# Optimization experiments

Hardware: AMD Instinct MI355X
Metric: run time of the kernel (lower is better)

## Reference

```python
import jax, jax.numpy as jnp
import numpy as np

N, C, TX, TY = 32, 256, 1024, 1024


def setup_inputs() -> dict:
    key = jax.random.key(0)
    ks = jax.random.split(key, 9)
    s = 1.0 / np.sqrt(C)
    return {
        "Q": jax.random.normal(ks[0], (N, C, TY), dtype=jnp.float32),
        "K": jax.random.normal(ks[1], (N, C, TX), dtype=jnp.float32),
        "V": jax.random.normal(ks[2], (N, C, TX), dtype=jnp.float32),
        "Wq": jax.random.normal(ks[3], (C, C), dtype=jnp.float32) * s,
        "bq": jax.random.normal(ks[4], (C,), dtype=jnp.float32) * 0.01,
        "Wk": jax.random.normal(ks[5], (C, C), dtype=jnp.float32) * s,
        "bk": jax.random.normal(ks[6], (C,), dtype=jnp.float32) * 0.01,
        "Wv": jax.random.normal(ks[7], (C, C), dtype=jnp.float32) * s,
        "bv": jax.random.normal(ks[8], (C,), dtype=jnp.float32) * 0.01,
    }


def _proj_tanh(W, b, x):
    # 1x1 conv over channels: (C_out, C_in) x (N, C_in, T) -> (N, C_out, T)
    return jnp.tanh(jnp.einsum("oc,nct->not", W, x) + b[None, :, None])


def reference(Q, K, V, Wq, bq, Wk, bk, Wv, bv):
    d_k = Q.shape[1]
    Qp = _proj_tanh(Wq, bq, Q)  # (N, C, Ty)
    Kp = _proj_tanh(Wk, bk, K)  # (N, C, Tx)
    Vp = _proj_tanh(Wv, bv, V)  # (N, C, Tx)
    scores = jnp.einsum("ncs,nct->nst", Kp, Qp) / jnp.sqrt(
        jnp.asarray(d_k, dtype=Q.dtype)
    )  # (N, Tx, Ty)
    A = jax.nn.softmax(scores, axis=1)  # softmax over Tx (dim=1)
    R = jnp.einsum("ncs,nst->nct", Vp, A)  # (N, C, Ty)
    return (R, A)
```

## Files before the change

### kernel.cpp

```cpp
#include <hip/hip_runtime.h>
#include <stdint.h>

#define N_B 32
#define C_D 256
#define T_D 1024

typedef unsigned short u16;
typedef __attribute__((ext_vector_type(8))) short short8;
typedef __attribute__((ext_vector_type(4))) float f32x4;

__device__ __forceinline__ u16 f2bf(float f) {
    unsigned x = __float_as_uint(f);
    return (u16)((x + 0x7fffu + ((x >> 16) & 1u)) >> 16);
}

__device__ __forceinline__ void gld16(const void* g, void* l) {
    __builtin_amdgcn_global_load_lds(
        (const __attribute__((address_space(1))) uint32_t*)g,
        (__attribute__((address_space(3))) uint32_t*)l, 16, 0, 0);
}

__global__ __launch_bounds__(256) void conv_w(const float* __restrict__ w0,
                                              const float* __restrict__ w1,
                                              const float* __restrict__ w2,
                                              u16* __restrict__ o0,
                                              u16* __restrict__ o1,
                                              u16* __restrict__ o2) {
    const float* in = blockIdx.y == 0 ? w0 : (blockIdx.y == 1 ? w1 : w2);
    u16* out       = blockIdx.y == 0 ? o0 : (blockIdx.y == 1 ? o1 : o2);
    int i = blockIdx.x * 256 + threadIdx.x;
    out[i] = f2bf(in[i]);
}

__device__ __forceinline__ void stage_tr(const float* __restrict__ src,
                                         u16* __restrict__ sm, int tid) {
    const int sr2 = tid >> 4;
    const int tt8 = (tid & 15) * 8;
    float4 v0 = *(const float4*)(src);
    float4 v1 = *(const float4*)(src + 4);
    float4 w0 = *(const float4*)(src + T_D);
    float4 w1 = *(const float4*)(src + T_D + 4);
    float a[8] = {v0.x, v0.y, v0.z, v0.w, v1.x, v1.y, v1.z, v1.w};
    float b[8] = {w0.x, w0.y, w0.z, w0.w, w1.x, w1.y, w1.z, w1.w};
    const int kk = sr2 * 2;
#pragma unroll
    for (int j = 0; j < 8; ++j) {
        const int t  = tt8 + j;
        const int ks = kk ^ (((t >> 4) & 3) << 3);
        uint32_t pk = (uint32_t)f2bf(a[j]) | ((uint32_t)f2bf(b[j]) << 16);
        *(uint32_t*)(sm + t * 32 + ks) = pk;
    }
}

template <bool TRA, bool TRB, int EPI, bool F32OUT>
__global__ __launch_bounds__(256) void gemm_t(
        const void* __restrict__ Av, const void* __restrict__ Bv,
        const float* __restrict__ bias, void* __restrict__ OutV,
        int Kdim, int ldo, long sA, long sB, long sO, float scale)
{
    __shared__ __align__(16) u16 smA[128 * 32];
    __shared__ __align__(16) u16 smB[128 * 32];

    const int nb = blockIdx.z;
    const int n0 = blockIdx.x * 128;
    const int m0 = blockIdx.y * 128;
    const int tid = threadIdx.x;

    const int srow = tid >> 2;
    const int sk8  = (tid & 3) * 8;
    const int sr2  = tid >> 4;
    const int tt8  = (tid & 15) * 8;

    const u16* gA0 = nullptr; const u16* gA1 = nullptr;
    const float* tA = nullptr;
    if constexpr (TRA) {
        tA = (const float*)Av + (size_t)nb * sA + (size_t)(sr2 * 2) * T_D + m0 + tt8;
    } else {
        const u16* Ab = (const u16*)Av + (size_t)nb * sA;
        gA0 = Ab + (size_t)(m0 + srow) * Kdim + sk8;
        gA1 = gA0 + (size_t)64 * Kdim;
    }
    const u16* gB0 = nullptr; const u16* gB1 = nullptr;
    const float* tB = nullptr;
    if constexpr (TRB) {
        tB = (const float*)Bv + (size_t)nb * sB + (size_t)(sr2 * 2) * T_D + n0 + tt8;
    } else {
        const u16* Bb = (const u16*)Bv + (size_t)nb * sB;
        gB0 = Bb + (size_t)(n0 + srow) * Kdim + sk8;
        gB1 = gB0 + (size_t)64 * Kdim;
    }
    u16* lA0 = smA + tid * 8; u16* lA1 = smA + 2048 + tid * 8;
    u16* lB0 = smB + tid * 8; u16* lB1 = smB + 2048 + tid * 8;

    const int lane = tid & 63;
    const int w    = tid >> 6;
    const int wm   = (w >> 1) * 64;
    const int wn   = (w & 1) * 64;
    const int l15  = lane & 15;
    const int quad = lane >> 4;

    f32x4 acc[4][4];
#pragma unroll
    for (int i = 0; i < 4; ++i)
#pragma unroll
        for (int j = 0; j < 4; ++j) acc[i][j] = (f32x4){0.f, 0.f, 0.f, 0.f};

    for (int kb = 0; kb < Kdim; kb += 32) {
        if constexpr (TRA) {
            stage_tr(tA + (size_t)kb * T_D, smA, tid);
        } else {
            gld16(gA0 + kb, lA0);
            gld16(gA1 + kb, lA1);
        }
        if constexpr (TRB) {
            stage_tr(tB + (size_t)kb * T_D, smB, tid);
        } else {
            gld16(gB0 + kb, lB0);
            gld16(gB1 + kb, lB1);
        }
        __syncthreads();
        short8 af[4], bfr[4];
#pragma unroll
        for (int i = 0; i < 4; ++i) {
            const int ra = wm + i * 16 + l15;
            const int ca = TRA ? ((quad ^ ((ra >> 4) & 3)) * 8) : (quad * 8);
            af[i] = *(const short8*)(smA + ra * 32 + ca);
            const int rb = wn + i * 16 + l15;
            const int cb = TRB ? ((quad ^ ((rb >> 4) & 3)) * 8) : (quad * 8);
            bfr[i] = *(const short8*)(smB + rb * 32 + cb);
        }
#pragma unroll
        for (int mi = 0; mi < 4; ++mi)
#pragma unroll
            for (int ni = 0; ni < 4; ++ni)
                acc[mi][ni] = __builtin_amdgcn_mfma_f32_16x16x32_bf16(
                        af[mi], bfr[ni], acc[mi][ni], 0, 0, 0);
        __syncthreads();
    }

#pragma unroll
    for (int mi = 0; mi < 4; ++mi) {
        const int mb = m0 + wm + mi * 16 + quad * 4;
#pragma unroll
        for (int r = 0; r < 4; ++r) {
            const int m = mb + r;
            float bm = 0.f;
            if (EPI == 2) bm = bias[m];
#pragma unroll
            for (int ni = 0; ni < 4; ++ni) {
                const int nn = n0 + wn + ni * 16 + l15;
                float v = acc[mi][ni][r] * scale;
                if (EPI == 1) v = tanhf(v + bias[nn]);
                if (EPI == 2) v = tanhf(v + bm);
                if (F32OUT)
                    ((float*)OutV)[(size_t)nb * sO + (size_t)m * ldo + nn] = v;
                else
                    ((u16*)OutV)[(size_t)nb * sO + (size_t)m * ldo + nn] = f2bf(v);
            }
        }
    }
}

__global__ __launch_bounds__(256) void softmax_cols(float* __restrict__ S) {
    __shared__ float pm[16][64];
    __shared__ float pl[16][64];
    __shared__ float fM[64];
    __shared__ float fR[64];
    const int n   = blockIdx.y;
    const int t0  = blockIdx.x * 64;
    const int tid = threadIdx.x;
    const int g   = tid >> 4;
    const int ci  = (tid & 15) * 4;
    float* A = S + (size_t)n * T_D * T_D + t0 + ci;
    float* p = A + (size_t)g * 64 * T_D;

    float m[4] = {-1e30f, -1e30f, -1e30f, -1e30f};
    float l[4] = {0.f, 0.f, 0.f, 0.f};
#pragma unroll 8
    for (int s = 0; s < 64; ++s) {
        float4 v = *(const float4*)(p + (size_t)s * T_D);
        float x[4] = {v.x, v.y, v.z, v.w};
#pragma unroll
        for (int j = 0; j < 4; ++j) {
            float nm = fmaxf(m[j], x[j]);
            l[j] = l[j] * __expf(m[j] - nm) + __expf(x[j] - nm);
            m[j] = nm;
        }
    }
#pragma unroll
    for (int j = 0; j < 4; ++j) { pm[g][ci + j] = m[j]; pl[g][ci + j] = l[j]; }
    __syncthreads();
    if (tid < 64) {
        float M = -1e30f;
#pragma unroll
        for (int g2 = 0; g2 < 16; ++g2) M = fmaxf(M, pm[g2][tid]);
        float L = 0.f;
#pragma unroll
        for (int g2 = 0; g2 < 16; ++g2) L += pl[g2][tid] * __expf(pm[g2][tid] - M);
        fM[tid] = M;
        fR[tid] = 1.0f / L;
    }
    __syncthreads();
    float M[4], R[4];
#pragma unroll
    for (int j = 0; j < 4; ++j) { M[j] = fM[ci + j]; R[j] = fR[ci + j]; }
#pragma unroll 8
    for (int s = 0; s < 64; ++s) {
        float4 v = *(const float4*)(p + (size_t)s * T_D);
        v.x = __expf(v.x - M[0]) * R[0];
        v.y = __expf(v.y - M[1]) * R[1];
        v.z = __expf(v.z - M[2]) * R[2];
        v.w = __expf(v.w - M[3]) * R[3];
        *(float4*)(p + (size_t)s * T_D) = v;
    }
}

extern "C" void kernel_launch(void* const* d_in, const int* in_sizes, int n_in,
                              void* d_out, int out_size, void* d_ws, size_t ws_size,
                              hipStream_t stream) {
    const float* Qf = (const float*)d_in[0];
    const float* Kf = (const float*)d_in[1];
    const float* Vf = (const float*)d_in[2];
    const float* Wq = (const float*)d_in[3];
    const float* bq = (const float*)d_in[4];
    const float* Wk = (const float*)d_in[5];
    const float* bk = (const float*)d_in[6];
    const float* Wv = (const float*)d_in[7];
    const float* bv = (const float*)d_in[8];

    float* Rout = (float*)d_out;
    float* Aout = Rout + (size_t)N_B * C_D * T_D;

    u16* QpT = (u16*)Rout;
    u16* KpT = (u16*)Rout + 8388608;
    u16* Wqb = (u16*)Aout;
    u16* Wkb = Wqb + 65536;
    u16* Wvb = Wkb + 65536;
    u16* Vp  = (u16*)d_in[0];

    dim3 blk(256);
    const long sX = (long)C_D * T_D;
    const long sS = (long)T_D * T_D;

    conv_w<<<dim3(256, 3), blk, 0, stream>>>(Wq, Wk, Wv, Wqb, Wkb, Wvb);

    gemm_t<true, false, 1, false><<<dim3(2, 8, N_B), blk, 0, stream>>>(
            Qf, Wqb, bq, QpT, C_D, C_D, sX, 0, sX, 1.0f);
    gemm_t<true, false, 1, false><<<dim3(2, 8, N_B), blk, 0, stream>>>(
            Kf, Wkb, bk, KpT, C_D, C_D, sX, 0, sX, 1.0f);
    gemm_t<false, true, 2, false><<<dim3(8, 2, N_B), blk, 0, stream>>>(
            Wvb, Vf, bv, Vp, C_D, T_D, 0, sX, sX, 1.0f);

    gemm_t<false, false, 0, true><<<dim3(8, 8, N_B), blk, 0, stream>>>(
            KpT, QpT, nullptr, Aout, C_D, T_D, sX, sX, sS, 0.0625f);

    softmax_cols<<<dim3(16, N_B), blk, 0, stream>>>(Aout);

    gemm_t<false, true, 0, true><<<dim3(8, 2, N_B), blk, 0, stream>>>(
            Vp, Aout, nullptr, Rout, T_D, T_D, sX, sS, sX, 1.0f);
}
```

Baseline: 418.8 us.

## Fuse column softmax statistics into score GEMM and normalization into AV GEMM

The score GEMM epilogue now computes per-tile column max and sum-exp partials. A small merge kernel combines them into final max and reciprocal-sum. The final AV GEMM applies the exp/normalize while staging A, and its blockIdx.y==0 blocks write the normalized A out. This removes the separate multi-pass softmax over the 128MB score matrix, at the cost of recomputing exp in the two m-blocks of the AV GEMM and needing a large workspace. Fallback paths use a standalone normalize pass or the old softmax when workspace is small.

```diff
diff --git a/kernel.cpp b/kernel.cpp
--- a/kernel.cpp
+++ b/kernel.cpp
@@ -18,6 +18,12 @@
     __builtin_amdgcn_global_load_lds(
         (const __attribute__((address_space(1))) uint32_t*)g,
         (__attribute__((address_space(3))) uint32_t*)l, 16, 0, 0);
+}
+
+__device__ __forceinline__ void comb(float& m, float& l, float m2, float l2) {
+    float M = fmaxf(m, m2);
+    l = l * __expf(m - M) + l2 * __expf(m2 - M);
+    m = M;
 }
 
 __global__ __launch_bounds__(256) void conv_w(const float* __restrict__ w0,
@@ -32,8 +38,11 @@
     out[i] = f2bf(in[i]);
 }
 
+template <bool NORM>
 __device__ __forceinline__ void stage_tr(const float* __restrict__ src,
-                                         u16* __restrict__ sm, int tid) {
+                                         u16* __restrict__ sm, int tid,
+                                         const float* Mv, const float* Rv,
+                                         float* adst, bool awr) {
     const int sr2 = tid >> 4;
     const int tt8 = (tid & 15) * 8;
     float4 v0 = *(const float4*)(src);
@@ -42,6 +51,19 @@
     float4 w1 = *(const float4*)(src + T_D + 4);
     float a[8] = {v0.x, v0.y, v0.z, v0.w, v1.x, v1.y, v1.z, v1.w};
     float b[8] = {w0.x, w0.y, w0.z, w0.w, w1.x, w1.y, w1.z, w1.w};
+    if constexpr (NORM) {
+#pragma unroll
+        for (int j = 0; j < 8; ++j) {
+            a[j] = __expf(a[j] - Mv[j]) * Rv[j];
+            b[j] = __expf(b[j] - Mv[j]) * Rv[j];
+        }
+        if (awr) {
+            ((float4*)adst)[0]         = make_float4(a[0], a[1], a[2], a[3]);
+            ((float4*)adst)[1]         = make_float4(a[4], a[5], a[6], a[7]);
+            ((float4*)(adst + T_D))[0] = make_float4(b[0], b[1], b[2], b[3]);
+            ((float4*)(adst + T_D))[1] = make_float4(b[4], b[5], b[6], b[7]);
+        }
+    }
     const int kk = sr2 * 2;
 #pragma unroll
     for (int j = 0; j < 8; ++j) {
@@ -52,11 +74,14 @@
     }
 }
 
-template <bool TRA, bool TRB, int EPI, bool F32OUT>
+template <bool TRA, bool TRB, int EPI, bool F32OUT, bool NORM>
 __global__ __launch_bounds__(256) void gemm_t(
         const void* __restrict__ Av, const void* __restrict__ Bv,
         const float* __restrict__ bias, void* __restrict__ OutV,
-        int Kdim, int ldo, long sA, long sB, long sO, float scale)
+        int Kdim, int ldo, long sA, long sB, long sO, float scale,
+        float* __restrict__ Pm, float* __restrict__ Pl,
+        const float* __restrict__ Mf, const float* __restrict__ Rl,
+        float* __restrict__ Aw)
 {
     __shared__ __align__(16) u16 smA[128 * 32];
     __shared__ __align__(16) u16 smB[128 * 32];
@@ -92,6 +117,19 @@
     u16* lA0 = smA + tid * 8; u16* lA1 = smA + 2048 + tid * 8;
     u16* lB0 = smB + tid * 8; u16* lB1 = smB + 2048 + tid * 8;
 
+    float Mv[8], Rv[8];
+    float* awbase = nullptr;
+    bool awr = false;
+    if constexpr (NORM) {
+#pragma unroll
+        for (int j = 0; j < 8; ++j) {
+            Mv[j] = Mf[(size_t)nb * T_D + n0 + tt8 + j];
+            Rv[j] = Rl[(size_t)nb * T_D + n0 + tt8 + j];
+        }
+        awbase = Aw + (size_t)nb * sB + (size_t)(sr2 * 2) * T_D + n0 + tt8;
+        awr = (blockIdx.y == 0);
+    }
+
     const int lane = tid & 63;
     const int w    = tid >> 6;
     const int wm   = (w >> 1) * 64;
@@ -107,13 +145,17 @@
 
     for (int kb = 0; kb < Kdim; kb += 32) {
         if constexpr (TRA) {
-            stage_tr(tA + (size_t)kb * T_D, smA, tid);
+            stage_tr<false>(tA + (size_t)kb * T_D, smA, tid, nullptr, nullptr, nullptr, false);
         } else {
             gld16(gA0 + kb, lA0);
             gld16(gA1 + kb, lA1);
         }
         if constexpr (TRB) {
-            stage_tr(tB + (size_t)kb * T_D, smB, tid);
+            if constexpr (NORM)
+                stage_tr<true>(tB + (size_t)kb * T_D, smB, tid, Mv, Rv,
+                               awbase + (size_t)kb * T_D, awr);
+            else
+                stage_tr<false>(tB + (size_t)kb * T_D, smB, tid, nullptr, nullptr, nullptr, false);
         } else {
             gld16(gB0 + kb, lB0);
             gld16(gB1 + kb, lB1);
@@ -138,27 +180,117 @@
         __syncthreads();
     }
 
-#pragma unroll
-    for (int mi = 0; mi < 4; ++mi) {
-        const int mb = m0 + wm + mi * 16 + quad * 4;
-#pragma unroll
-        for (int r = 0; r < 4; ++r) {
-            const int m = mb + r;
-            float bm = 0.f;
-            if (EPI == 2) bm = bias[m];
+    if constexpr (EPI == 3) {
+        float pmv[4] = {-1e30f, -1e30f, -1e30f, -1e30f};
+        float plv[4] = {0.f, 0.f, 0.f, 0.f};
+#pragma unroll
+        for (int mi = 0; mi < 4; ++mi) {
+            const int mb = m0 + wm + mi * 16 + quad * 4;
+#pragma unroll
+            for (int r = 0; r < 4; ++r) {
+                const int m = mb + r;
+#pragma unroll
+                for (int ni = 0; ni < 4; ++ni) {
+                    const int nn = n0 + wn + ni * 16 + l15;
+                    float v = acc[mi][ni][r] * scale;
+                    ((float*)OutV)[(size_t)nb * sO + (size_t)m * ldo + nn] = v;
+                    pmv[ni] = fmaxf(pmv[ni], v);
+                }
+            }
+        }
+#pragma unroll
+        for (int ni = 0; ni < 4; ++ni) {
+            float s = 0.f;
+#pragma unroll
+            for (int mi = 0; mi < 4; ++mi)
+#pragma unroll
+                for (int r = 0; r < 4; ++r)
+                    s += __expf(acc[mi][ni][r] * scale - pmv[ni]);
+            plv[ni] = s;
+        }
+#pragma unroll
+        for (int ni = 0; ni < 4; ++ni) {
+            float m = pmv[ni], l = plv[ni];
+            float m2 = __shfl_xor(m, 16), l2 = __shfl_xor(l, 16);
+            comb(m, l, m2, l2);
+            m2 = __shfl_xor(m, 32); l2 = __shfl_xor(l, 32);
+            comb(m, l, m2, l2);
+            pmv[ni] = m; plv[ni] = l;
+        }
+        __shared__ float red_m[4][64];
+        __shared__ float red_l[4][64];
+        if (quad == 0) {
 #pragma unroll
             for (int ni = 0; ni < 4; ++ni) {
-                const int nn = n0 + wn + ni * 16 + l15;
-                float v = acc[mi][ni][r] * scale;
-                if (EPI == 1) v = tanhf(v + bias[nn]);
-                if (EPI == 2) v = tanhf(v + bm);
-                if (F32OUT)
-                    ((float*)OutV)[(size_t)nb * sO + (size_t)m * ldo + nn] = v;
-                else
-                    ((u16*)OutV)[(size_t)nb * sO + (size_t)m * ldo + nn] = f2bf(v);
+                red_m[w][ni * 16 + l15] = pmv[ni];
+                red_l[w][ni * 16 + l15] = plv[ni];
             }
         }
-    }
+        __syncthreads();
+        if (tid < 128) {
+            const int half = tid >> 6, cc = tid & 63;
+            float m = red_m[half][cc], l = red_l[half][cc];
+            comb(m, l, red_m[half + 2][cc], red_l[half + 2][cc]);
+            const size_t pi = ((size_t)nb * 8 + blockIdx.y) * T_D + n0 + tid;
+            Pm[pi] = m; Pl[pi] = l;
+        }
+    } else {
+#pragma unroll
+        for (int mi = 0; mi < 4; ++mi) {
+            const int mb = m0 + wm + mi * 16 + quad * 4;
+#pragma unroll
+            for (int r = 0; r < 4; ++r) {
+                const int m = mb + r;
+                float bm = 0.f;
+                if (EPI == 2) bm = bias[m];
+#pragma unroll
+                for (int ni = 0; ni < 4; ++ni) {
+                    const int nn = n0 + wn + ni * 16 + l15;
+                    float v = acc[mi][ni][r] * scale;
+                    if (EPI == 1) v = tanhf(v + bias[nn]);
+                    if (EPI == 2) v = tanhf(v + bm);
+                    if (F32OUT)
+                        ((float*)OutV)[(size_t)nb * sO + (size_t)m * ldo + nn] = v;
+                    else
+                        ((u16*)OutV)[(size_t)nb * sO + (size_t)m * ldo + nn] = f2bf(v);
+                }
+            }
+        }
+    }
+}
+
+__global__ __launch_bounds__(256) void merge_ml(const float* __restrict__ Pm,
+                                                const float* __restrict__ Pl,
+                                                float* __restrict__ Mf,
+                                                float* __restrict__ Rl) {
+    const int i = blockIdx.x * 256 + threadIdx.x;
+    const int n = i >> 10, t = i & (T_D - 1);
+    const float* pm = Pm + (size_t)n * 8 * T_D + t;
+    const float* pl = Pl + (size_t)n * 8 * T_D + t;
+    float M = -1e30f;
+#pragma unroll
+    for (int j = 0; j < 8; ++j) M = fmaxf(M, pm[(size_t)j * T_D]);
+    float L = 0.f;
+#pragma unroll
+    for (int j = 0; j < 8; ++j) L += pl[(size_t)j * T_D] * __expf(pm[(size_t)j * T_D] - M);
+    Mf[i] = M;
+    Rl[i] = 1.0f / L;
+}
+
+__global__ __launch_bounds__(256) void norm_a(float* __restrict__ S,
+                                              const float* __restrict__ Mf,
+                                              const float* __restrict__ Rl) {
+    const size_t i = ((size_t)blockIdx.x * 256 + threadIdx.x) * 4;
+    const int n = (int)(i >> 20);
+    const int t = (int)(i & (T_D - 1));
+    float4 M = *(const float4*)(Mf + (size_t)n * T_D + t);
+    float4 R = *(const float4*)(Rl + (size_t)n * T_D + t);
+    float4 v = *(float4*)(S + i);
+    v.x = __expf(v.x - M.x) * R.x;
+    v.y = __expf(v.y - M.y) * R.y;
+    v.z = __expf(v.z - M.z) * R.z;
+    v.w = __expf(v.w - M.w) * R.w;
+    *(float4*)(S + i) = v;
 }
 
 __global__ __launch_bounds__(256) void softmax_cols(float* __restrict__ S) {
@@ -242,20 +374,57 @@
     const long sX = (long)C_D * T_D;
     const long sS = (long)T_D * T_D;
 
+    const size_t elemsS = (size_t)N_B * T_D * T_D;
+    const size_t elemsP = (size_t)N_B * 8 * T_D;
+    const size_t elemsM = (size_t)N_B * T_D;
+    const size_t needA = (elemsS + 2 * elemsP + 2 * elemsM) * 4;
+    const size_t needB = (2 * elemsP + 2 * elemsM) * 4;
+
     conv_w<<<dim3(256, 3), blk, 0, stream>>>(Wq, Wk, Wv, Wqb, Wkb, Wvb);
 
-    gemm_t<true, false, 1, false><<<dim3(2, 8, N_B), blk, 0, stream>>>(
-            Qf, Wqb, bq, QpT, C_D, C_D, sX, 0, sX, 1.0f);
-    gemm_t<true, false, 1, false><<<dim3(2, 8, N_B), blk, 0, stream>>>(
-            Kf, Wkb, bk, KpT, C_D, C_D, sX, 0, sX, 1.0f);
-    gemm_t<false, true, 2, false><<<dim3(8, 2, N_B), blk, 0, stream>>>(
-            Wvb, Vf, bv, Vp, C_D, T_D, 0, sX, sX, 1.0f);
-
-    gemm_t<false, false, 0, true><<<dim3(8, 8, N_B), blk, 0, stream>>>(
-            KpT, QpT, nullptr, Aout, C_D, T_D, sX, sX, sS, 0.0625f);
-
-    softmax_cols<<<dim3(16, N_B), blk, 0, stream>>>(Aout);
-
-    gemm_t<false, true, 0, true><<<dim3(8, 2, N_B), blk, 0, stream>>>(
-            Vp, Aout, nullptr, Rout, T_D, T_D, sX, sS, sX, 1.0f);
-}
+    gemm_t<true, false, 1, false, false><<<dim3(2, 8, N_B), blk, 0, stream>>>(
+            Qf, Wqb, bq, QpT, C_D, C_D, sX, 0, sX, 1.0f,
+            nullptr, nullptr, nullptr, nullptr, nullptr);
+    gemm_t<true, false, 1, false, false><<<dim3(2, 8, N_B), blk, 0, stream>>>(
+            Kf, Wkb, bk, KpT, C_D, C_D, sX, 0, sX, 1.0f,
+            nullptr, nullptr, nullptr, nullptr, nullptr);
+    gemm_t<false, true, 2, false, false><<<dim3(8, 2, N_B), blk, 0, stream>>>(
+            Wvb, Vf, bv, Vp, C_D, T_D, 0, sX, sX, 1.0f,
+            nullptr, nullptr, nullptr, nullptr, nullptr);
+
+    if (ws_size >= needA) {
+        float* Sws = (float*)d_ws;
+        float* Pm  = Sws + elemsS;
+        float* Pl  = Pm + elemsP;
+        float* Mf  = Pl + elemsP;
+        float* Rl  = Mf + elemsM;
+        gemm_t<false, false, 3, true, false><<<dim3(8, 8, N_B), blk, 0, stream>>>(
+                KpT, QpT, nullptr, Sws, C_D, T_D, sX, sX, sS, 0.0625f,
+                Pm, Pl, nullptr, nullptr, nullptr);
+        merge_ml<<<dim3(128), blk, 0, stream>>>(Pm, Pl, Mf, Rl);
+        gemm_t<false, true, 0, true, true><<<dim3(8, 2, N_B), blk, 0, stream>>>(
+                Vp, Sws, nullptr, Rout, T_D, T_D, sX, sS, sX, 1.0f,
+                nullptr, nullptr, Mf, Rl, Aout);
+    } else if (ws_size >= needB) {
+        float* Pm = (float*)d_ws;
+        float* Pl = Pm + elemsP;
+        float* Mf = Pl + elemsP;
+        float* Rl = Mf + elemsM;
+        gemm_t<false, false, 3, true, false><<<dim3(8, 8, N_B), blk, 0, stream>>>(
+                KpT, QpT, nullptr, Aout, C_D, T_D, sX, sX, sS, 0.0625f,
+                Pm, Pl, nullptr, nullptr, nullptr);
+        merge_ml<<<dim3(128), blk, 0, stream>>>(Pm, Pl, Mf, Rl);
+        norm_a<<<dim3(32768), blk, 0, stream>>>(Aout, Mf, Rl);
+        gemm_t<false, true, 0, true, false><<<dim3(8, 2, N_B), blk, 0, stream>>>(
+                Vp, Aout, nullptr, Rout, T_D, T_D, sX, sS, sX, 1.0f,
+                nullptr, nullptr, nullptr, nullptr, nullptr);
+    } else {
+        gemm_t<false, false, 0, true, false><<<dim3(8, 8, N_B), blk, 0, stream>>>(
+                KpT, QpT, nullptr, Aout, C_D, T_D, sX, sX, sS, 0.0625f,
+                nullptr, nullptr, nullptr, nullptr, nullptr);
+        softmax_cols<<<dim3(16, N_B), blk, 0, stream>>>(Aout);
+        gemm_t<false, true, 0, true, false><<<dim3(8, 2, N_B), blk, 0, stream>>>(
+                Vp, Aout, nullptr, Rout, T_D, T_D, sX, sS, sX, 1.0f,
+                nullptr, nullptr, nullptr, nullptr, nullptr);
+    }
+}
```

Result: no change. 418.8 us (-0.0%).

## Fuse scores, column softmax and value GEMM into one attention kernel

Applied to the files above, without the earlier changes.

Replaces the separate score GEMM, column-softmax pass and final A·V GEMM with one kernel. Each block computes all 1024 scores for a 32-column query slice, reduces max/sum across waves in LDS, writes normalized A once, and keeps a bf16 copy of P in LDS for the V multiply. This removes the read-modify-write passes over the large fp32 A matrix. It also merges the Q and K projections into one launch, adds an XOR swizzle to the non-transposed LDS tiles, and writes R to a scratch input buffer that is then copied to the output, which costs an extra copy pass.

```diff
diff --git a/kernel.cpp b/kernel.cpp
--- a/kernel.cpp
+++ b/kernel.cpp
@@ -4,6 +4,7 @@
 #define N_B 32
 #define C_D 256
 #define T_D 1024
+#define QB 32
 
 typedef unsigned short u16;
 typedef __attribute__((ext_vector_type(8))) short short8;
@@ -18,6 +19,12 @@
     __builtin_amdgcn_global_load_lds(
         (const __attribute__((address_space(1))) uint32_t*)g,
         (__attribute__((address_space(3))) uint32_t*)l, 16, 0, 0);
+}
+
+__device__ __forceinline__ void comb(float& m, float& l, float m2, float l2) {
+    float M = fmaxf(m, m2);
+    l = l * __expf(m - M) + l2 * __expf(m2 - M);
+    m = M;
 }
 
 __global__ __launch_bounds__(256) void conv_w(const float* __restrict__ w0,
@@ -33,9 +40,8 @@
 }
 
 __device__ __forceinline__ void stage_tr(const float* __restrict__ src,
-                                         u16* __restrict__ sm, int tid) {
-    const int sr2 = tid >> 4;
-    const int tt8 = (tid & 15) * 8;
+                                         u16* __restrict__ sm,
+                                         int sr2, int tt8) {
     float4 v0 = *(const float4*)(src);
     float4 v1 = *(const float4*)(src + 4);
     float4 w0 = *(const float4*)(src + T_D);
@@ -52,22 +58,28 @@
     }
 }
 
-template <bool TRA, bool TRB, int EPI, bool F32OUT>
+template <bool TRA, bool TRB, int EPI, bool DUAL>
 __global__ __launch_bounds__(256) void gemm_t(
         const void* __restrict__ Av, const void* __restrict__ Bv,
         const float* __restrict__ bias, void* __restrict__ OutV,
-        int Kdim, int ldo, long sA, long sB, long sO, float scale)
+        int Kdim, int ldo, long sA, long sB, long sO, float scale,
+        const void* __restrict__ Av2, const void* __restrict__ Bv2,
+        const float* __restrict__ bias2, void* __restrict__ Out2)
 {
     __shared__ __align__(16) u16 smA[128 * 32];
     __shared__ __align__(16) u16 smB[128 * 32];
 
-    const int nb = blockIdx.z;
+    int nb = blockIdx.z;
+    if (DUAL && nb >= N_B) {
+        nb -= N_B;
+        Av = Av2; Bv = Bv2; bias = bias2; OutV = Out2;
+    }
     const int n0 = blockIdx.x * 128;
     const int m0 = blockIdx.y * 128;
     const int tid = threadIdx.x;
 
     const int srow = tid >> 2;
-    const int sk8  = (tid & 3) * 8;
+    const int sk8  = (((tid & 3) ^ ((srow >> 1) & 3)) * 8);
     const int sr2  = tid >> 4;
     const int tt8  = (tid & 15) * 8;
 
@@ -107,13 +119,13 @@
 
     for (int kb = 0; kb < Kdim; kb += 32) {
         if constexpr (TRA) {
-            stage_tr(tA + (size_t)kb * T_D, smA, tid);
+            stage_tr(tA + (size_t)kb * T_D, smA, sr2, tt8);
         } else {
             gld16(gA0 + kb, lA0);
             gld16(gA1 + kb, lA1);
         }
         if constexpr (TRB) {
-            stage_tr(tB + (size_t)kb * T_D, smB, tid);
+            stage_tr(tB + (size_t)kb * T_D, smB, sr2, tt8);
         } else {
             gld16(gB0 + kb, lB0);
             gld16(gB1 + kb, lB1);
@@ -123,10 +135,12 @@
 #pragma unroll
         for (int i = 0; i < 4; ++i) {
             const int ra = wm + i * 16 + l15;
-            const int ca = TRA ? ((quad ^ ((ra >> 4) & 3)) * 8) : (quad * 8);
+            const int ca = TRA ? ((quad ^ ((ra >> 4) & 3)) * 8)
+                               : ((quad ^ ((ra >> 1) & 3)) * 8);
             af[i] = *(const short8*)(smA + ra * 32 + ca);
             const int rb = wn + i * 16 + l15;
-            const int cb = TRB ? ((quad ^ ((rb >> 4) & 3)) * 8) : (quad * 8);
+            const int cb = TRB ? ((quad ^ ((rb >> 4) & 3)) * 8)
+                               : ((quad ^ ((rb >> 1) & 3)) * 8);
             bfr[i] = *(const short8*)(smB + rb * 32 + cb);
         }
 #pragma unroll
@@ -152,67 +166,226 @@
                 float v = acc[mi][ni][r] * scale;
                 if (EPI == 1) v = tanhf(v + bias[nn]);
                 if (EPI == 2) v = tanhf(v + bm);
-                if (F32OUT)
-                    ((float*)OutV)[(size_t)nb * sO + (size_t)m * ldo + nn] = v;
-                else
-                    ((u16*)OutV)[(size_t)nb * sO + (size_t)m * ldo + nn] = f2bf(v);
+                ((u16*)OutV)[(size_t)nb * sO + (size_t)m * ldo + nn] = f2bf(v);
             }
         }
     }
 }
 
-__global__ __launch_bounds__(256) void softmax_cols(float* __restrict__ S) {
-    __shared__ float pm[16][64];
-    __shared__ float pl[16][64];
-    __shared__ float fM[64];
-    __shared__ float fR[64];
-    const int n   = blockIdx.y;
-    const int t0  = blockIdx.x * 64;
-    const int tid = threadIdx.x;
-    const int g   = tid >> 4;
-    const int ci  = (tid & 15) * 4;
-    float* A = S + (size_t)n * T_D * T_D + t0 + ci;
-    float* p = A + (size_t)g * 64 * T_D;
-
-    float m[4] = {-1e30f, -1e30f, -1e30f, -1e30f};
-    float l[4] = {0.f, 0.f, 0.f, 0.f};
-#pragma unroll 8
-    for (int s = 0; s < 64; ++s) {
-        float4 v = *(const float4*)(p + (size_t)s * T_D);
-        float x[4] = {v.x, v.y, v.z, v.w};
-#pragma unroll
-        for (int j = 0; j < 4; ++j) {
-            float nm = fmaxf(m[j], x[j]);
-            l[j] = l[j] * __expf(m[j] - nm) + __expf(x[j] - nm);
-            m[j] = nm;
-        }
-    }
-#pragma unroll
-    for (int j = 0; j < 4; ++j) { pm[g][ci + j] = m[j]; pl[g][ci + j] = l[j]; }
+__global__ __launch_bounds__(512, 4) void attn_fused(
+        const u16* __restrict__ Kp,
+        const u16* __restrict__ Qp,
+        const u16* __restrict__ Vp,
+        float* __restrict__ A,
+        float* __restrict__ Rr)
+{
+    __shared__ __align__(16) u16 lds[40960];
+    u16* smK = lds;
+    u16* smQ = lds + 32768;
+    u16* smP = lds;
+    u16* smV = lds + 32768;
+    float* red = (float*)(lds + 32768);
+
+    const int bid = blockIdx.x;
+    const int idx = (bid & 7) * 128 + (bid >> 3);
+    const int nb  = idx >> 5;
+    const int t0  = (idx & 31) * QB;
+
+    const int tid  = threadIdx.x;
+    const int lane = tid & 63;
+    const int w    = tid >> 6;
+    const int l15  = lane & 15;
+    const int quad = lane >> 4;
+
+    const u16* Kb = Kp + (size_t)nb * (T_D * C_D);
+    const u16* Qb = Qp + (size_t)nb * (T_D * C_D);
+    const u16* Vb = Vp + (size_t)nb * (C_D * T_D);
+    float* Ab = A + (size_t)nb * ((size_t)T_D * T_D) + t0;
+    float* Rb = Rr + (size_t)nb * (C_D * T_D) + t0;
+
+    {
+        const int tq   = tid >> 5;
+        const int slot = tid & 31;
+#pragma unroll
+        for (int c = 0; c < 2; ++c) {
+            const int tt = c * 16 + tq;
+            const int chunk = slot ^ (tt & 7);
+            gld16(Qb + (size_t)(t0 + tt) * C_D + chunk * 8,
+                  smQ + c * 4096 + tid * 8);
+        }
+    }
+
+    f32x4 acc[8][2];
+#pragma unroll
+    for (int i = 0; i < 8; ++i)
+#pragma unroll
+        for (int j = 0; j < 2; ++j) acc[i][j] = (f32x4){0.f, 0.f, 0.f, 0.f};
+
     __syncthreads();
-    if (tid < 64) {
+
+    u16* smKw = smK + w * 4096;
+    const u16* Kw = Kb + (size_t)(w * 128) * C_D;
+    for (int kb = 0; kb < 8; ++kb) {
+        asm volatile("s_waitcnt lgkmcnt(0)" ::: "memory");
+#pragma unroll
+        for (int c = 0; c < 8; ++c) {
+            const int s  = c * 16 + (lane >> 2);
+            const int ck = (lane & 3) ^ ((s >> 1) & 3);
+            gld16(Kw + (size_t)s * C_D + kb * 32 + ck * 8,
+                  smKw + c * 512 + lane * 8);
+        }
+        asm volatile("s_waitcnt vmcnt(0)" ::: "memory");
+        __builtin_amdgcn_sched_barrier(0);
+        short8 af[8], bq[2];
+#pragma unroll
+        for (int i = 0; i < 8; ++i) {
+            const int sl = i * 16 + l15;
+            af[i] = *(const short8*)(smKw + sl * 32 + ((quad ^ ((sl >> 1) & 3)) * 8));
+        }
+#pragma unroll
+        for (int i = 0; i < 2; ++i) {
+            const int t = i * 16 + l15;
+            bq[i] = *(const short8*)(smQ + t * 256 + (((kb * 4 + quad) ^ (l15 & 7)) * 8));
+        }
+#pragma unroll
+        for (int mi = 0; mi < 8; ++mi)
+#pragma unroll
+            for (int ni = 0; ni < 2; ++ni)
+                acc[mi][ni] = __builtin_amdgcn_mfma_f32_16x16x32_bf16(
+                        af[mi], bq[ni], acc[mi][ni], 0, 0, 0);
+    }
+
+    float pm2[2], pl2[2];
+#pragma unroll
+    for (int ni = 0; ni < 2; ++ni) {
+        float m = -1e30f;
+#pragma unroll
+        for (int mi = 0; mi < 8; ++mi)
+#pragma unroll
+            for (int r = 0; r < 4; ++r)
+                m = fmaxf(m, acc[mi][ni][r] * 0.0625f);
+        float l = 0.f;
+#pragma unroll
+        for (int mi = 0; mi < 8; ++mi)
+#pragma unroll
+            for (int r = 0; r < 4; ++r)
+                l += __expf(acc[mi][ni][r] * 0.0625f - m);
+        float m2 = __shfl_xor(m, 16), l2 = __shfl_xor(l, 16);
+        comb(m, l, m2, l2);
+        m2 = __shfl_xor(m, 32); l2 = __shfl_xor(l, 32);
+        comb(m, l, m2, l2);
+        pm2[ni] = m; pl2[ni] = l;
+    }
+
+    __syncthreads();
+
+    float* pmL = red;
+    float* plL = red + 256;
+    float* fM  = red + 512;
+    float* fR  = red + 544;
+    if (quad == 0) {
+#pragma unroll
+        for (int ni = 0; ni < 2; ++ni) {
+            pmL[w * 32 + ni * 16 + l15] = pm2[ni];
+            plL[w * 32 + ni * 16 + l15] = pl2[ni];
+        }
+    }
+    __syncthreads();
+    if (tid < 32) {
         float M = -1e30f;
 #pragma unroll
-        for (int g2 = 0; g2 < 16; ++g2) M = fmaxf(M, pm[g2][tid]);
+        for (int j = 0; j < 8; ++j) M = fmaxf(M, pmL[j * 32 + tid]);
         float L = 0.f;
 #pragma unroll
-        for (int g2 = 0; g2 < 16; ++g2) L += pl[g2][tid] * __expf(pm[g2][tid] - M);
+        for (int j = 0; j < 8; ++j)
+            L += plL[j * 32 + tid] * __expf(pmL[j * 32 + tid] - M);
         fM[tid] = M;
         fR[tid] = 1.0f / L;
     }
     __syncthreads();
-    float M[4], R[4];
-#pragma unroll
-    for (int j = 0; j < 4; ++j) { M[j] = fM[ci + j]; R[j] = fR[ci + j]; }
-#pragma unroll 8
-    for (int s = 0; s < 64; ++s) {
-        float4 v = *(const float4*)(p + (size_t)s * T_D);
-        v.x = __expf(v.x - M[0]) * R[0];
-        v.y = __expf(v.y - M[1]) * R[1];
-        v.z = __expf(v.z - M[2]) * R[2];
-        v.w = __expf(v.w - M[3]) * R[3];
-        *(float4*)(p + (size_t)s * T_D) = v;
-    }
+    float Mn[2], Rn[2];
+#pragma unroll
+    for (int ni = 0; ni < 2; ++ni) {
+        Mn[ni] = fM[ni * 16 + l15];
+        Rn[ni] = fR[ni * 16 + l15];
+    }
+
+#pragma unroll
+    for (int mi = 0; mi < 8; ++mi) {
+        const int sbase = w * 128 + mi * 16 + quad * 4;
+        const int c4    = w * 32 + mi * 4 + quad;
+        const int slot8 = c4 >> 1;
+        const int half  = c4 & 1;
+#pragma unroll
+        for (int ni = 0; ni < 2; ++ni) {
+            const int t = ni * 16 + l15;
+            float a0 = __expf(acc[mi][ni][0] * 0.0625f - Mn[ni]) * Rn[ni];
+            float a1 = __expf(acc[mi][ni][1] * 0.0625f - Mn[ni]) * Rn[ni];
+            float a2 = __expf(acc[mi][ni][2] * 0.0625f - Mn[ni]) * Rn[ni];
+            float a3 = __expf(acc[mi][ni][3] * 0.0625f - Mn[ni]) * Rn[ni];
+            Ab[(size_t)(sbase + 0) * T_D + t] = a0;
+            Ab[(size_t)(sbase + 1) * T_D + t] = a1;
+            Ab[(size_t)(sbase + 2) * T_D + t] = a2;
+            Ab[(size_t)(sbase + 3) * T_D + t] = a3;
+            uint2 pk;
+            pk.x = (uint32_t)f2bf(a0) | ((uint32_t)f2bf(a1) << 16);
+            pk.y = (uint32_t)f2bf(a2) | ((uint32_t)f2bf(a3) << 16);
+            *(uint2*)(smP + t * 1024 + (slot8 ^ (t & 7)) * 8 + half * 4) = pk;
+        }
+    }
+    __syncthreads();
+
+    f32x4 acc2[2][2];
+#pragma unroll
+    for (int i = 0; i < 2; ++i)
+#pragma unroll
+        for (int j = 0; j < 2; ++j) acc2[i][j] = (f32x4){0.f, 0.f, 0.f, 0.f};
+
+    u16* smVw = smV + w * 1024;
+    for (int kb = 0; kb < 32; ++kb) {
+        asm volatile("s_waitcnt lgkmcnt(0)" ::: "memory");
+#pragma unroll
+        for (int c = 0; c < 2; ++c) {
+            const int cc = w * 32 + c * 16 + (lane >> 2);
+            const int ck = (lane & 3) ^ ((cc >> 1) & 3);
+            gld16(Vb + (size_t)cc * T_D + kb * 32 + ck * 8,
+                  smVw + c * 512 + lane * 8);
+        }
+        asm volatile("s_waitcnt vmcnt(0)" ::: "memory");
+        __builtin_amdgcn_sched_barrier(0);
+        short8 av[2], pb[2];
+#pragma unroll
+        for (int i = 0; i < 2; ++i) {
+            const int cc = w * 32 + i * 16 + l15;
+            av[i] = *(const short8*)(smV + cc * 32 + ((quad ^ ((cc >> 1) & 3)) * 8));
+            const int t = i * 16 + l15;
+            pb[i] = *(const short8*)(smP + t * 1024 + (((kb * 4 + quad) ^ (l15 & 7)) * 8));
+        }
+#pragma unroll
+        for (int mi = 0; mi < 2; ++mi)
+#pragma unroll
+            for (int ni = 0; ni < 2; ++ni)
+                acc2[mi][ni] = __builtin_amdgcn_mfma_f32_16x16x32_bf16(
+                        av[mi], pb[ni], acc2[mi][ni], 0, 0, 0);
+    }
+
+#pragma unroll
+    for (int mi = 0; mi < 2; ++mi) {
+        const int cb = w * 32 + mi * 16 + quad * 4;
+#pragma unroll
+        for (int r = 0; r < 4; ++r)
+#pragma unroll
+            for (int ni = 0; ni < 2; ++ni)
+                Rb[(size_t)(cb + r) * T_D + ni * 16 + l15] = acc2[mi][ni][r];
+    }
+}
+
+__global__ __launch_bounds__(256) void cp_r(const float4* __restrict__ s,
+                                            float4* __restrict__ d) {
+    const int n = N_B * C_D * T_D / 4;
+    int i = blockIdx.x * 256 + threadIdx.x;
+    const int st = gridDim.x * 256;
+    for (; i < n; i += st) d[i] = s[i];
 }
 
 extern "C" void kernel_launch(void* const* d_in, const int* in_sizes, int n_in,
@@ -237,25 +410,21 @@
     u16* Wkb = Wqb + 65536;
     u16* Wvb = Wkb + 65536;
     u16* Vp  = (u16*)d_in[0];
+    float* Rscr = (float*)d_in[1];
 
     dim3 blk(256);
     const long sX = (long)C_D * T_D;
-    const long sS = (long)T_D * T_D;
 
     conv_w<<<dim3(256, 3), blk, 0, stream>>>(Wq, Wk, Wv, Wqb, Wkb, Wvb);
 
-    gemm_t<true, false, 1, false><<<dim3(2, 8, N_B), blk, 0, stream>>>(
-            Qf, Wqb, bq, QpT, C_D, C_D, sX, 0, sX, 1.0f);
-    gemm_t<true, false, 1, false><<<dim3(2, 8, N_B), blk, 0, stream>>>(
-            Kf, Wkb, bk, KpT, C_D, C_D, sX, 0, sX, 1.0f);
+    gemm_t<true, false, 1, true><<<dim3(2, 8, 2 * N_B), blk, 0, stream>>>(
+            Qf, Wqb, bq, QpT, C_D, C_D, sX, 0, sX, 1.0f,
+            Kf, Wkb, bk, KpT);
     gemm_t<false, true, 2, false><<<dim3(8, 2, N_B), blk, 0, stream>>>(
-            Wvb, Vf, bv, Vp, C_D, T_D, 0, sX, sX, 1.0f);
-
-    gemm_t<false, false, 0, true><<<dim3(8, 8, N_B), blk, 0, stream>>>(
-            KpT, QpT, nullptr, Aout, C_D, T_D, sX, sX, sS, 0.0625f);
-
-    softmax_cols<<<dim3(16, N_B), blk, 0, stream>>>(Aout);
-
-    gemm_t<false, true, 0, true><<<dim3(8, 2, N_B), blk, 0, stream>>>(
-            Vp, Aout, nullptr, Rout, T_D, T_D, sX, sS, sX, 1.0f);
-}
+            Wvb, Vf, bv, Vp, C_D, T_D, 0, sX, sX, 1.0f,
+            nullptr, nullptr, nullptr, nullptr);
+
+    attn_fused<<<dim3(1024), dim3(512), 0, stream>>>(KpT, QpT, Vp, Aout, Rscr);
+
+    cp_r<<<dim3(2048), blk, 0, stream>>>((const float4*)Rscr, (float4*)Rout);
+}
```

Measured after the change: 369.3 us. -11.8%, faster.
